# Kernel optimization log

Measured on AMD Instinct MI355X. Metric: run time of the kernel, lower is better.

## Reference

```python
import jax, jax.numpy as jnp
import numpy as np

B, H, W, C, HEADS, WS, SS = 32, 56, 56, 512, 16, 7, 3
HID = 4 * C
N = WS * WS          # tokens per window = 49
NW = (H // WS) * (W // WS)  # windows per image = 64
HD = C // HEADS
SCALE = HD ** -0.5

def _rel_index():
    coords = np.stack(np.meshgrid(np.arange(WS), np.arange(WS), indexing='ij'))
    cf = coords.reshape(2, -1)
    rel = (cf[:, :, None] - cf[:, None, :]).transpose(1, 2, 0)
    rel[..., 0] += WS - 1
    rel[..., 1] += WS - 1
    rel[..., 0] *= 2 * WS - 1
    return rel.sum(-1)  # [N, N]

REL_IDX = _rel_index()

def _attn_mask():
    # standard Swin SW-MSA mask: label 3x3 shifted regions, diff labels -> -100
    img = np.zeros((H, W), dtype=np.float32)
    cnt = 0
    for hs in (slice(0, -WS), slice(-WS, -SS), slice(-SS, None)):
        for ws_ in (slice(0, -WS), slice(-WS, -SS), slice(-SS, None)):
            img[hs, ws_] = cnt
            cnt += 1
    mw = img.reshape(H // WS, WS, W // WS, WS).transpose(0, 2, 1, 3).reshape(NW, N)
    diff = mw[:, None, :] - mw[:, :, None]
    return jnp.asarray(np.where(diff != 0, -100.0, 0.0).astype(np.float32))  # [NW, N, N]

ATTN_MASK = _attn_mask()

def layernorm(x, g, b, eps=1e-5):
    m = jnp.mean(x, -1, keepdims=True)
    v = jnp.mean((x - m) ** 2, -1, keepdims=True)
    return (x - m) * jax.lax.rsqrt(v + eps) * g + b

def setup_inputs():
    key = jax.random.key(0)
    ks = jax.random.split(key, 8)
    f32 = jnp.float32
    return {
        'x': jax.random.normal(ks[0], (B, H * W, C), f32),
        'norm1_g': jnp.ones((C,), f32), 'norm1_b': jnp.zeros((C,), f32),
        'qkv_w': jax.random.normal(ks[1], (3 * C, C), f32) * 0.02,
        'qkv_b': jnp.zeros((3 * C,), f32),
        'rel_bias': jax.random.normal(ks[2], ((2 * WS - 1) ** 2, HEADS), f32) * 0.02,
        'proj_w': jax.random.normal(ks[3], (C, C), f32) * 0.02,
        'proj_b': jnp.zeros((C,), f32),
        'norm2_g': jnp.ones((C,), f32), 'norm2_b': jnp.zeros((C,), f32),
        'mlp_w1': jax.random.normal(ks[4], (HID, C), f32) * 0.02,
        'mlp_b1': jnp.zeros((HID,), f32),
        'mlp_w2': jax.random.normal(ks[5], (C, HID), f32) * 0.02,
        'mlp_b2': jnp.zeros((C,), f32),
    }

def reference(x, norm1_g, norm1_b, qkv_w, qkv_b, rel_bias, proj_w, proj_b,
              norm2_g, norm2_b, mlp_w1, mlp_b1, mlp_w2, mlp_b2):
    skip = x
    h = layernorm(x, norm1_g, norm1_b).reshape(B, H, W, C)
    h = jnp.roll(h, (-SS, -SS), axis=(1, 2))  # cyclic shift
    # window partition -> [B*NW, N, C]
    h = h.reshape(B, H // WS, WS, W // WS, WS, C).transpose(0, 1, 3, 2, 4, 5).reshape(B * NW, N, C)
    qkv = (h @ qkv_w.T + qkv_b).reshape(B * NW, N, 3, HEADS, HD).transpose(2, 0, 3, 1, 4)
    q, k, v = qkv[0] * SCALE, qkv[1], qkv[2]  # [B*NW, HEADS, N, HD]
    attn = jnp.einsum('whnd,whmd->whnm', q, k)
    bias = rel_bias[REL_IDX.reshape(-1)].reshape(N, N, HEADS).transpose(2, 0, 1)
    attn = attn + bias[None]
    attn = attn.reshape(B, NW, HEADS, N, N) + ATTN_MASK[None, :, None]
    attn = jax.nn.softmax(attn, axis=-1).reshape(B * NW, HEADS, N, N)
    h = jnp.einsum('whnm,whmd->whnd', attn, v).transpose(0, 2, 1, 3).reshape(B * NW, N, C)
    h = h @ proj_w.T + proj_b
    # window reverse + reverse cyclic shift
    h = h.reshape(B, H // WS, W // WS, WS, WS, C).transpose(0, 1, 3, 2, 4, 5).reshape(B, H, W, C)
    h = jnp.roll(h, (SS, SS), axis=(1, 2)).reshape(B, H * W, C)
    x = skip + h
    m = layernorm(x, norm2_g, norm2_b)
    m = jax.nn.gelu(m @ mlp_w1.T + mlp_b1, approximate=False) @ mlp_w2.T + mlp_b2
    return x + m
```

## Files before the change

kernel.cpp:

```cpp
#include <hip/hip_runtime.h>
#include <cstdint>
#include <cstddef>

#define DI __device__ __forceinline__

typedef __bf16 bf16_t;
typedef __bf16 bf16x8 __attribute__((ext_vector_type(8)));
typedef float f32x4 __attribute__((ext_vector_type(4)));

static constexpr float SCALE = 0.17677669529663687f;

DI bf16_t f2b(float f) {
  uint32_t u = __builtin_bit_cast(uint32_t, f);
  u += 0x7fffu + ((u >> 16) & 1u);
  return __builtin_bit_cast(bf16_t, (uint16_t)(u >> 16));
}

DI void gld16(const void* g, void* l) {
  __builtin_amdgcn_global_load_lds(
      (const __attribute__((address_space(1))) uint32_t*)g,
      (__attribute__((address_space(3))) uint32_t*)l, 16, 0, 0);
}

__global__ __launch_bounds__(256)
void cvtw(const float* __restrict__ in, bf16_t* __restrict__ out, int n) {
  int i = (blockIdx.x * 256 + threadIdx.x) * 4;
  if (i >= n) return;
  float4 v = *(const float4*)(in + i);
  ushort4 o;
  o.x = __builtin_bit_cast(uint16_t, f2b(v.x));
  o.y = __builtin_bit_cast(uint16_t, f2b(v.y));
  o.z = __builtin_bit_cast(uint16_t, f2b(v.z));
  o.w = __builtin_bit_cast(uint16_t, f2b(v.w));
  *(ushort4*)(out + i) = o;
}

__global__ __launch_bounds__(256)
void bias_pre(const float* __restrict__ rel, float* __restrict__ bf) {
  int idx = blockIdx.x * 256 + threadIdx.x;
  int head = idx >> 12, t1 = (idx >> 6) & 63, t2 = idx & 63;
  float v = -1e30f;
  if (t1 < 49 && t2 < 49) {
    int i1 = t1 / 7, j1 = t1 - i1 * 7, i2 = t2 / 7, j2 = t2 - i2 * 7;
    v = rel[((i1 - i2 + 6) * 13 + (j1 - j2 + 6)) * 16 + head];
  }
  bf[idx] = v;
}

template<bool WIN>
__global__ __launch_bounds__(128)
void ln_kernel(const float* __restrict__ in, const float* __restrict__ g,
               const float* __restrict__ be, bf16_t* __restrict__ out)
{
  const int r = blockIdx.x;
  const int tid = threadIdx.x;
  long srow;
  if (WIN) {
    int bw = r / 49, t = r - bw * 49;
    int b = bw >> 6, w = bw & 63;
    int wh = w >> 3, ww = w & 7;
    int i = t / 7, j = t - i * 7;
    int hs = wh * 7 + i + 3; if (hs >= 56) hs -= 56;
    int wsr = ww * 7 + j + 3; if (wsr >= 56) wsr -= 56;
    srow = (long)b * 3136 + hs * 56 + wsr;
  } else {
    srow = r;
  }
  const float4 v = *(const float4*)(in + srow * 512 + tid * 4);
  float s = v.x + v.y + v.z + v.w;
  float sq = v.x * v.x + v.y * v.y + v.z * v.z + v.w * v.w;
#pragma unroll
  for (int m = 1; m < 64; m <<= 1) { s += __shfl_xor(s, m); sq += __shfl_xor(sq, m); }
  __shared__ float ls[2], lq[2];
  if ((tid & 63) == 0) { ls[tid >> 6] = s; lq[tid >> 6] = sq; }
  __syncthreads();
  s = ls[0] + ls[1]; sq = lq[0] + lq[1];
  const float mean = s * (1.f / 512.f);
  const float rs = rsqrtf(sq * (1.f / 512.f) - mean * mean + 1e-5f);
  const float4 gg = *(const float4*)(g + tid * 4);
  const float4 bb = *(const float4*)(be + tid * 4);
  ushort4 o;
  o.x = __builtin_bit_cast(uint16_t, f2b((v.x - mean) * rs * gg.x + bb.x));
  o.y = __builtin_bit_cast(uint16_t, f2b((v.y - mean) * rs * gg.y + bb.y));
  o.z = __builtin_bit_cast(uint16_t, f2b((v.z - mean) * rs * gg.z + bb.z));
  o.w = __builtin_bit_cast(uint16_t, f2b((v.w - mean) * rs * gg.w + bb.w));
  *(ushort4*)(out + (long)r * 512 + tid * 4) = o;
}

#define MFMA16(a, b, c) __builtin_amdgcn_mfma_f32_16x16x32_bf16((a), (b), (c), 0, 0, 0)

template<int EPI>
__global__ __launch_bounds__(512, 2)
void gemm256(const bf16_t* __restrict__ A, const bf16_t* __restrict__ Bw,
             const float* __restrict__ bias, const float* __restrict__ extra,
             void* __restrict__ out0, void* __restrict__ out1v, void* __restrict__ out2v,
             const int K, const int NBN)
{
  __shared__ __align__(128) bf16_t lds[8][8192];
  const int tid = threadIdx.x, lane = tid & 63, wave = tid >> 6;
  const int NT = K >> 6;
  const int ntiles = NBN * 392;

  const int xcd = blockIdx.x & 7, sidx = blockIdx.x >> 3;
  const int c = xcd * 32 + sidx;
  const int q2 = ntiles >> 8, r2 = ntiles & 255;
  const int t0 = c * q2 + (c < r2 ? c : r2);
  const int t1 = t0 + q2 + (c < r2 ? 1 : 0);

  const int srow = tid >> 2, slot = tid & 3;
  const int chunk = slot ^ ((srow >> 1) & 3);
  const size_t rowK = (size_t)128 * K;
  const size_t PANEL = (size_t)256 * K;

  int bmC = t0 / NBN, bnC = t0 - bmC * NBN;

  const bf16_t* pAs = A + (size_t)(bmC * 256 + srow) * K + chunk * 8;
  const bf16_t* pBs = Bw + (size_t)(bnC * 256 + srow) * K + chunk * 8;
  int hA = 0, hB = 0, ktA = 0, hhA = 0, bnA = bnC, ktB = 0, hhB = 0, bnB = bnC;
  const int ST = (t1 - t0) * NT;
  const int hEnd = ST * 2;

#define STG_A() do { \
    if (hA < hEnd) { \
      const bf16_t* _p = pAs + ktA * 64 + hhA * 32; \
      bf16_t* _l = &lds[(ktA & 1) * 2 + hhA][tid * 8]; \
      gld16(_p, _l); gld16(_p + rowK, _l + 4096); \
      ++hA; hhA ^= 1; \
      if (!hhA) { if (++ktA == NT) { ktA = 0; if (++bnA == NBN) { bnA = 0; pAs += PANEL; } } } \
    } \
  } while (0)

#define STG_B() do { \
    if (hB < hEnd) { \
      const bf16_t* _p = pBs + ktB * 64 + hhB * 32; \
      bf16_t* _l = &lds[4 + (ktB & 1) * 2 + hhB][tid * 8]; \
      gld16(_p, _l); gld16(_p + rowK, _l + 4096); \
      ++hB; hhB ^= 1; \
      if (!hhB) { if (++ktB == NT) { ktB = 0; pBs += PANEL; if (++bnB == NBN) { bnB = 0; pBs -= (size_t)NBN * PANEL; } } } \
    } \
  } while (0)

  const int fr = lane & 15, fkc = lane >> 4;
  const int wr = wave >> 2, wc = wave & 3;
  const int slotq = (fkc ^ ((fr >> 1) & 3)) << 3;
  const int aoff = (wr * 128 + fr) * 32 + slotq;
  const int boff = (wc * 64 + fr) * 32 + slotq;

  f32x4 acc[8][4] = {};
  bf16x8 af[8], bq[4];

  STG_A(); STG_B(); STG_A(); STG_B(); STG_A(); STG_B(); STG_A();
  asm volatile("s_waitcnt vmcnt(6)");
  __builtin_amdgcn_s_barrier();
  __builtin_amdgcn_sched_barrier(0);

#define PH_SYNC() \
  __builtin_amdgcn_sched_barrier(0); \
  __builtin_amdgcn_s_barrier(); \
  asm volatile("s_waitcnt lgkmcnt(0)"); \
  __builtin_amdgcn_sched_barrier(0); \
  __builtin_amdgcn_s_setprio(1)

#define PH_END() \
  __builtin_amdgcn_s_setprio(0); \
  __builtin_amdgcn_sched_barrier(0); \
  __builtin_amdgcn_s_barrier()

#define MM2(N0, N1) \
  _Pragma("unroll") \
  for (int m = 0; m < 8; ++m) { \
    acc[m][N0] = MFMA16(af[m], bq[N0], acc[m][N0]); \
    acc[m][N1] = MFMA16(af[m], bq[N1], acc[m][N1]); \
  }

#define KTILE(B) do { \
     \
    _Pragma("unroll") \
    for (int m = 0; m < 8; ++m) af[m] = *(const bf16x8*)&lds[(B) * 2][aoff + m * 512]; \
    bq[0] = *(const bf16x8*)&lds[4 + (B) * 2][boff]; \
    bq[1] = *(const bf16x8*)&lds[4 + (B) * 2][boff + 512]; \
    STG_B(); \
    PH_SYNC(); \
    MM2(0, 1); \
    PH_END(); \
     \
    bq[2] = *(const bf16x8*)&lds[4 + (B) * 2][boff + 1024]; \
    bq[3] = *(const bf16x8*)&lds[4 + (B) * 2][boff + 1536]; \
    STG_A(); \
    PH_SYNC(); \
    MM2(2, 3); \
    PH_END(); \
     \
    _Pragma("unroll") \
    for (int m = 0; m < 8; ++m) af[m] = *(const bf16x8*)&lds[(B) * 2 + 1][aoff + m * 512]; \
    bq[0] = *(const bf16x8*)&lds[4 + (B) * 2 + 1][boff]; \
    bq[1] = *(const bf16x8*)&lds[4 + (B) * 2 + 1][boff + 512]; \
    STG_B(); \
    PH_SYNC(); \
    MM2(0, 1); \
    PH_END(); \
     \
    bq[2] = *(const bf16x8*)&lds[4 + (B) * 2 + 1][boff + 1024]; \
    bq[3] = *(const bf16x8*)&lds[4 + (B) * 2 + 1][boff + 1536]; \
    STG_A(); \
    PH_SYNC(); \
    MM2(2, 3); \
    __builtin_amdgcn_s_setprio(0); \
    __builtin_amdgcn_sched_barrier(0); \
    if (sG + 2 < ST) asm volatile("s_waitcnt vmcnt(6)"); \
    else             asm volatile("s_waitcnt vmcnt(0)"); \
    __builtin_amdgcn_s_barrier(); \
    __builtin_amdgcn_sched_barrier(0); \
    ++sG; \
  } while (0)

  int sG = 0;
  const int rq = fkc * 4;
  for (int t = t0; t < t1; ++t) {
#pragma unroll 1
    for (int k2 = 0; k2 < NT; k2 += 2) {
      KTILE(0);
      KTILE(1);
    }
    {
      float bs[4];
#pragma unroll
      for (int n = 0; n < 4; ++n) bs[n] = bias[bnC * 256 + wc * 64 + n * 16 + fr];
#pragma unroll
      for (int m = 0; m < 8; ++m) {
#pragma unroll
        for (int j = 0; j < 4; ++j) {
          const int grow = bmC * 256 + wr * 128 + m * 16 + rq + j;
          long obase = 0;
          if (EPI == 0) {
            int bwi = grow / 49, t_ = grow - bwi * 49;
            obase = ((long)bwi * 784 + t_) * 32;
          } else if (EPI == 1) {
            int bwi = grow / 49, t_ = grow - bwi * 49;
            int b = bwi >> 6, w = bwi & 63;
            int wh = w >> 3, ww = w & 7;
            int i = t_ / 7, jj = t_ - i * 7;
            int hs = wh * 7 + i + 3; if (hs >= 56) hs -= 56;
            int wsr = ww * 7 + jj + 3; if (wsr >= 56) wsr -= 56;
            obase = ((long)b * 3136 + hs * 56 + wsr) * 512;
          } else if (EPI == 2) {
            obase = (long)grow * 2048;
          } else {
            obase = (long)grow * 512;
          }
#pragma unroll
          for (int n = 0; n < 4; ++n) {
            const int gcol = bnC * 256 + wc * 64 + n * 16 + fr;
            float v = acc[m][n][j] + bs[n];
            if (EPI == 0) {
              int part = gcol >> 9, head = (gcol >> 5) & 15, d = gcol & 31;
              if (part == 0) v *= SCALE;
              bf16_t* dst = (bf16_t*)(part == 0 ? out0 : (part == 1 ? out1v : out2v));
              dst[obase + (long)head * 1568 + d] = f2b(v);
            } else if (EPI == 1) {
              ((float*)out0)[obase + gcol] = v + extra[obase + gcol];
            } else if (EPI == 2) {
              float m2 = v * v;
              float z = v * fmaf(0.07135481627f, m2, 1.59576912161f);
              float e = __expf(z);
              float rr = __builtin_amdgcn_rcpf(e + 1.0f);
              ((bf16_t*)out0)[obase + gcol] = f2b(fmaf(-v, rr, v));
            } else {
              ((float*)out0)[obase + gcol] = v + extra[obase + gcol];
            }
          }
        }
      }
#pragma unroll
      for (int m = 0; m < 8; ++m)
#pragma unroll
        for (int n = 0; n < 4; ++n) acc[m][n] = (f32x4){0.f, 0.f, 0.f, 0.f};
    }
    if (++bnC == NBN) { bnC = 0; ++bmC; }
  }
#undef KTILE
#undef MM2
#undef PH_END
#undef PH_SYNC
#undef STG_A
#undef STG_B
}

__global__ __launch_bounds__(256)
void attn_kernel(const bf16_t* __restrict__ qb, const bf16_t* __restrict__ kb,
                 const bf16_t* __restrict__ vb, const float* __restrict__ biasf,
                 bf16_t* __restrict__ aout)
{
  __shared__ bf16_t Q[64 * 32];
  __shared__ bf16_t Kl[64 * 32];
  __shared__ bf16_t Vt[32 * 64];
  __shared__ bf16_t Pl[4][16 * 64];
  const int bid = blockIdx.x;
  const int bw = bid >> 4, head = bid & 15;
  const int tid = threadIdx.x, lane = tid & 63, wave = tid >> 6;
  {
    uint4 z = {0u, 0u, 0u, 0u};
    *(uint4*)&Q[tid * 8] = z;
    *(uint4*)&Kl[tid * 8] = z;
    *(uint4*)&Vt[tid * 8] = z;
  }
  __syncthreads();
  const bf16_t* qsrc = qb + (long)bid * (49 * 32);
  const bf16_t* ksrc = kb + (long)bid * (49 * 32);
  const bf16_t* vsrc = vb + (long)bid * (49 * 32);
  if (tid < 196) {
    *(uint4*)&Q[tid * 8] = *(const uint4*)(qsrc + tid * 8);
    *(uint4*)&Kl[tid * 8] = *(const uint4*)(ksrc + tid * 8);
  }
  for (int e = tid; e < 1568; e += 256) {
    int t = e >> 5, d = e & 31;
    Vt[d * 64 + t] = vsrc[e];
  }
  __syncthreads();
  const int fr = lane & 15, fk = (lane >> 4) * 8, rq = (lane >> 4) * 4;
  bf16x8 aq = *(const bf16x8*)&Q[(wave * 16 + fr) * 32 + fk];
  f32x4 s[4];
#pragma unroll
  for (int n = 0; n < 4; ++n) {
    bf16x8 bk = *(const bf16x8*)&Kl[(n * 16 + fr) * 32 + fk];
    f32x4 z = {0.f, 0.f, 0.f, 0.f};
    s[n] = __builtin_amdgcn_mfma_f32_16x16x32_bf16(aq, bk, z, 0, 0, 0);
  }
  const int w = bw & 63;
  const bool wh7 = ((w >> 3) == 7), ww7 = ((w & 7) == 7);
  const float* bh = biasf + head * 4096;
#pragma unroll
  for (int j = 0; j < 4; ++j) {
    const int row = wave * 16 + rq + j;
    int i1 = row / 7, j1 = row - i1 * 7;
    bool b1h = wh7 && (i1 >= 4), b1w = ww7 && (j1 >= 4);
    float pv[4];
    float mx = -3.0e38f;
#pragma unroll
    for (int n = 0; n < 4; ++n) {
      const int col = n * 16 + fr;
      float v = s[n][j] + bh[row * 64 + col];
      if (wh7 || ww7) {
        int i2 = col / 7, j2 = col - i2 * 7;
        bool b2h = wh7 && (i2 >= 4), b2w = ww7 && (j2 >= 4);
        if ((b1h != b2h) || (b1w != b2w)) v -= 100.f;
      }
      pv[n] = v;
      mx = fmaxf(mx, v);
    }
#pragma unroll
    for (int msk = 1; msk < 16; msk <<= 1) mx = fmaxf(mx, __shfl_xor(mx, msk));
    float sm = 0.f;
#pragma unroll
    for (int n = 0; n < 4; ++n) { pv[n] = __expf(pv[n] - mx); sm += pv[n]; }
#pragma unroll
    for (int msk = 1; msk < 16; msk <<= 1) sm += __shfl_xor(sm, msk);
    const float inv = 1.f / sm;
#pragma unroll
    for (int n = 0; n < 4; ++n)
      Pl[wave][(rq + j) * 64 + n * 16 + fr] = f2b(pv[n] * inv);
  }
  __syncthreads();
  f32x4 o[2] = {};
#pragma unroll
  for (int kk = 0; kk < 2; ++kk) {
    bf16x8 pa = *(const bf16x8*)&Pl[wave][fr * 64 + kk * 32 + fk];
#pragma unroll
    for (int dt = 0; dt < 2; ++dt) {
      bf16x8 vv = *(const bf16x8*)&Vt[(dt * 16 + fr) * 64 + kk * 32 + fk];
      o[dt] = __builtin_amdgcn_mfma_f32_16x16x32_bf16(pa, vv, o[dt], 0, 0, 0);
    }
  }
#pragma unroll
  for (int j = 0; j < 4; ++j) {
    const int t1 = wave * 16 + rq + j;
    if (t1 < 49) {
      bf16_t* dst = aout + ((long)bw * 49 + t1) * 512 + head * 32;
      dst[fr] = f2b(o[0][j]);
      dst[16 + fr] = f2b(o[1][j]);
    }
  }
}

extern "C" void kernel_launch(void* const* d_in, const int* in_sizes, int n_in,
                              void* d_out, int out_size, void* d_ws, size_t ws_size,
                              hipStream_t stream)
{
  const float* x      = (const float*)d_in[0];
  const float* n1g    = (const float*)d_in[1];
  const float* n1b    = (const float*)d_in[2];
  const float* qkv_w  = (const float*)d_in[3];
  const float* qkv_b  = (const float*)d_in[4];
  const float* rel    = (const float*)d_in[5];
  const float* proj_w = (const float*)d_in[6];
  const float* proj_b = (const float*)d_in[7];
  const float* n2g    = (const float*)d_in[8];
  const float* n2b    = (const float*)d_in[9];
  const float* w1     = (const float*)d_in[10];
  const float* b1     = (const float*)d_in[11];
  const float* w2     = (const float*)d_in[12];
  const float* b2     = (const float*)d_in[13];

  char* ws = (char*)d_ws;
  bf16_t* Wqkv  = (bf16_t*)(ws + 0);
  bf16_t* Wproj = (bf16_t*)(ws + 1572864);
  bf16_t* Wm1   = (bf16_t*)(ws + 2097152);
  bf16_t* Wm2   = (bf16_t*)(ws + 4194304);
  float*  biasf = (float*)(ws + 6291456);
  const size_t ABYTES = (size_t)100352 * 512 * 2;
  const size_t P1 = 8388608;
  const size_t P2 = P1 + ABYTES + 1048576;
  bf16_t* xw      = (bf16_t*)(ws + P1);
  bf16_t* qbuf    = (bf16_t*)(ws + P2);
  bf16_t* kbuf    = (bf16_t*)(ws + P2 + ABYTES);
  bf16_t* vbuf    = (bf16_t*)(ws + P2 + 2 * ABYTES);
  bf16_t* attnout = xw;
  bf16_t* h2      = xw;
  bf16_t* hidden  = qbuf;

  cvtw<<<768, 256, 0, stream>>>(qkv_w, Wqkv, 1536 * 512);
  cvtw<<<256, 256, 0, stream>>>(proj_w, Wproj, 512 * 512);
  cvtw<<<1024, 256, 0, stream>>>(w1, Wm1, 2048 * 512);
  cvtw<<<1024, 256, 0, stream>>>(w2, Wm2, 512 * 2048);
  bias_pre<<<256, 256, 0, stream>>>(rel, biasf);

  ln_kernel<true><<<100352, 128, 0, stream>>>(x, n1g, n1b, xw);
  gemm256<0><<<256, 512, 0, stream>>>(xw, Wqkv, qkv_b, nullptr,
                                      qbuf, kbuf, vbuf, 512, 6);
  attn_kernel<<<32768, 256, 0, stream>>>(qbuf, kbuf, vbuf, biasf, attnout);
  gemm256<1><<<256, 512, 0, stream>>>(attnout, Wproj, proj_b, x,
                                      d_out, nullptr, nullptr, 512, 2);
  ln_kernel<false><<<100352, 128, 0, stream>>>((const float*)d_out, n2g, n2b, h2);
  gemm256<2><<<256, 512, 0, stream>>>(h2, Wm1, b1, nullptr,
                                      hidden, nullptr, nullptr, 512, 8);
  gemm256<3><<<256, 512, 0, stream>>>(hidden, Wm2, b2, (const float*)d_out,
                                      d_out, nullptr, nullptr, 2048, 2);
}
```

Measured before the change: 1.410 ms.

## Assign GEMM tiles per XCD with fixed N-column per block for L2 reuse

Replaces the contiguous linear tile-range split with a scheme where each XCD owns 49 consecutive M-panels. Each block keeps a fixed N column and strides over M panels by G=32/NBN. Blocks on the same XCD therefore share A panels in that XCD's L2, and each block reuses one B panel, so the bias load is also hoisted out of the tile loop. The risk is idle blocks when 32 is not divisible by NBN, plus possibly coarser load balance.

```diff
diff --git a/kernel.cpp b/kernel.cpp
--- a/kernel.cpp
+++ b/kernel.cpp
@@ -99,26 +99,25 @@
   __shared__ __align__(128) bf16_t lds[8][8192];
   const int tid = threadIdx.x, lane = tid & 63, wave = tid >> 6;
   const int NT = K >> 6;
-  const int ntiles = NBN * 392;
-
-  const int xcd = blockIdx.x & 7, sidx = blockIdx.x >> 3;
-  const int c = xcd * 32 + sidx;
-  const int q2 = ntiles >> 8, r2 = ntiles & 255;
-  const int t0 = c * q2 + (c < r2 ? c : r2);
-  const int t1 = t0 + q2 + (c < r2 ? 1 : 0);
+
+  const int xcd = blockIdx.x & 7, j = blockIdx.x >> 3;
+  const int G = 32 / NBN;
+  if (j >= G * NBN) return;
+  const int bmo = j / NBN;
+  const int bn = j - bmo * NBN;
+  const int m0 = xcd * 49;
+  const int tiles = (49 - bmo + G - 1) / G;
+  const int ST = tiles * NT;
+  const int hEnd = 2 * ST;
 
   const int srow = tid >> 2, slot = tid & 3;
   const int chunk = slot ^ ((srow >> 1) & 3);
   const size_t rowK = (size_t)128 * K;
-  const size_t PANEL = (size_t)256 * K;
-
-  int bmC = t0 / NBN, bnC = t0 - bmC * NBN;
-
-  const bf16_t* pAs = A + (size_t)(bmC * 256 + srow) * K + chunk * 8;
-  const bf16_t* pBs = Bw + (size_t)(bnC * 256 + srow) * K + chunk * 8;
-  int hA = 0, hB = 0, ktA = 0, hhA = 0, bnA = bnC, ktB = 0, hhB = 0, bnB = bnC;
-  const int ST = (t1 - t0) * NT;
-  const int hEnd = ST * 2;
+  const size_t strideA = (size_t)G * 256 * K;
+
+  const bf16_t* pAs = A + ((size_t)(m0 + bmo) * 256 + srow) * K + chunk * 8;
+  const bf16_t* pBs = Bw + ((size_t)bn * 256 + srow) * K + chunk * 8;
+  int hA = 0, hB = 0, ktA = 0, hhA = 0, ktB = 0, hhB = 0;
 
 #define STG_A() do { \
     if (hA < hEnd) { \
@@ -126,7 +125,7 @@
       bf16_t* _l = &lds[(ktA & 1) * 2 + hhA][tid * 8]; \
       gld16(_p, _l); gld16(_p + rowK, _l + 4096); \
       ++hA; hhA ^= 1; \
-      if (!hhA) { if (++ktA == NT) { ktA = 0; if (++bnA == NBN) { bnA = 0; pAs += PANEL; } } } \
+      if (!hhA) { if (++ktA == NT) { ktA = 0; pAs += strideA; } } \
     } \
   } while (0)
 
@@ -136,7 +135,7 @@
       bf16_t* _l = &lds[4 + (ktB & 1) * 2 + hhB][tid * 8]; \
       gld16(_p, _l); gld16(_p + rowK, _l + 4096); \
       ++hB; hhB ^= 1; \
-      if (!hhB) { if (++ktB == NT) { ktB = 0; pBs += PANEL; if (++bnB == NBN) { bnB = 0; pBs -= (size_t)NBN * PANEL; } } } \
+      if (!hhB) { if (++ktB == NT) ktB = 0; }   \
     } \
   } while (0)
 
@@ -215,68 +214,68 @@
   } while (0)
 
   int sG = 0;
+  int bmC = m0 + bmo;
   const int rq = fkc * 4;
-  for (int t = t0; t < t1; ++t) {
+  float bs[4];
+#pragma unroll
+  for (int n = 0; n < 4; ++n) bs[n] = bias[bn * 256 + wc * 64 + n * 16 + fr];
+
+  for (int t = 0; t < tiles; ++t) {
 #pragma unroll 1
     for (int k2 = 0; k2 < NT; k2 += 2) {
       KTILE(0);
       KTILE(1);
     }
-    {
-      float bs[4];
-#pragma unroll
-      for (int n = 0; n < 4; ++n) bs[n] = bias[bnC * 256 + wc * 64 + n * 16 + fr];
-#pragma unroll
-      for (int m = 0; m < 8; ++m) {
-#pragma unroll
-        for (int j = 0; j < 4; ++j) {
-          const int grow = bmC * 256 + wr * 128 + m * 16 + rq + j;
-          long obase = 0;
+#pragma unroll
+    for (int m = 0; m < 8; ++m) {
+#pragma unroll
+      for (int jj4 = 0; jj4 < 4; ++jj4) {
+        const int grow = bmC * 256 + wr * 128 + m * 16 + rq + jj4;
+        long obase = 0;
+        if (EPI == 0) {
+          int bwi = grow / 49, t_ = grow - bwi * 49;
+          obase = ((long)bwi * 784 + t_) * 32;
+        } else if (EPI == 1) {
+          int bwi = grow / 49, t_ = grow - bwi * 49;
+          int b = bwi >> 6, w = bwi & 63;
+          int wh = w >> 3, ww = w & 7;
+          int i = t_ / 7, jj = t_ - i * 7;
+          int hs = wh * 7 + i + 3; if (hs >= 56) hs -= 56;
+          int wsr = ww * 7 + jj + 3; if (wsr >= 56) wsr -= 56;
+          obase = ((long)b * 3136 + hs * 56 + wsr) * 512;
+        } else if (EPI == 2) {
+          obase = (long)grow * 2048;
+        } else {
+          obase = (long)grow * 512;
+        }
+#pragma unroll
+        for (int n = 0; n < 4; ++n) {
+          const int gcol = bn * 256 + wc * 64 + n * 16 + fr;
+          float v = acc[m][n][jj4] + bs[n];
           if (EPI == 0) {
-            int bwi = grow / 49, t_ = grow - bwi * 49;
-            obase = ((long)bwi * 784 + t_) * 32;
+            int part = gcol >> 9, head = (gcol >> 5) & 15, d = gcol & 31;
+            if (part == 0) v *= SCALE;
+            bf16_t* dst = (bf16_t*)(part == 0 ? out0 : (part == 1 ? out1v : out2v));
+            dst[obase + (long)head * 1568 + d] = f2b(v);
           } else if (EPI == 1) {
-            int bwi = grow / 49, t_ = grow - bwi * 49;
-            int b = bwi >> 6, w = bwi & 63;
-            int wh = w >> 3, ww = w & 7;
-            int i = t_ / 7, jj = t_ - i * 7;
-            int hs = wh * 7 + i + 3; if (hs >= 56) hs -= 56;
-            int wsr = ww * 7 + jj + 3; if (wsr >= 56) wsr -= 56;
-            obase = ((long)b * 3136 + hs * 56 + wsr) * 512;
+            ((float*)out0)[obase + gcol] = v + extra[obase + gcol];
           } else if (EPI == 2) {
-            obase = (long)grow * 2048;
+            float m2 = v * v;
+            float z = v * fmaf(0.07135481627f, m2, 1.59576912161f);
+            float e = __expf(z);
+            float rr = __builtin_amdgcn_rcpf(e + 1.0f);
+            ((bf16_t*)out0)[obase + gcol] = f2b(fmaf(-v, rr, v));
           } else {
-            obase = (long)grow * 512;
-          }
-#pragma unroll
-          for (int n = 0; n < 4; ++n) {
-            const int gcol = bnC * 256 + wc * 64 + n * 16 + fr;
-            float v = acc[m][n][j] + bs[n];
-            if (EPI == 0) {
-              int part = gcol >> 9, head = (gcol >> 5) & 15, d = gcol & 31;
-              if (part == 0) v *= SCALE;
-              bf16_t* dst = (bf16_t*)(part == 0 ? out0 : (part == 1 ? out1v : out2v));
-              dst[obase + (long)head * 1568 + d] = f2b(v);
-            } else if (EPI == 1) {
-              ((float*)out0)[obase + gcol] = v + extra[obase + gcol];
-            } else if (EPI == 2) {
-              float m2 = v * v;
-              float z = v * fmaf(0.07135481627f, m2, 1.59576912161f);
-              float e = __expf(z);
-              float rr = __builtin_amdgcn_rcpf(e + 1.0f);
-              ((bf16_t*)out0)[obase + gcol] = f2b(fmaf(-v, rr, v));
-            } else {
-              ((float*)out0)[obase + gcol] = v + extra[obase + gcol];
-            }
+            ((float*)out0)[obase + gcol] = v + extra[obase + gcol];
           }
         }
       }
-#pragma unroll
-      for (int m = 0; m < 8; ++m)
-#pragma unroll
-        for (int n = 0; n < 4; ++n) acc[m][n] = (f32x4){0.f, 0.f, 0.f, 0.f};
     }
-    if (++bnC == NBN) { bnC = 0; ++bmC; }
+#pragma unroll
+    for (int m = 0; m < 8; ++m)
+#pragma unroll
+      for (int n = 0; n < 4; ++n) acc[m][n] = (f32x4){0.f, 0.f, 0.f, 0.f};
+    bmC += G;
   }
 #undef KTILE
 #undef MM2
```

After: 1.315 ms, median of 2. 6.7% less time.
